# Optimization experiments

Measured on AMD Instinct MI355X. Metric: run time of the kernel, lower is better.

Reference implementation:

```python
import jax, jax.numpy as jnp
import numpy as np

B_, L_, D_MODEL = 2, 2048, 1024
D_INNER, D_STATE, D_CONV, DT_RANK = 2048, 16, 4, 64


def setup_inputs() -> dict:
    key = jax.random.key(0)
    ks = jax.random.split(key, 8)
    hidden_states = jax.random.normal(ks[0], (B_, L_, D_MODEL), jnp.float32)
    in_proj_w = jax.random.normal(ks[1], (2 * D_INNER, D_MODEL), jnp.float32) * (D_MODEL ** -0.5)
    conv_w = jax.random.normal(ks[2], (D_INNER, 1, D_CONV), jnp.float32) * (D_CONV ** -0.5)
    conv_b = jnp.zeros((D_INNER,), jnp.float32)
    x_proj_w = jax.random.normal(ks[3], (DT_RANK + 2 * D_STATE, D_INNER), jnp.float32) * (D_INNER ** -0.5)
    dt_std = DT_RANK ** -0.5
    dt_proj_w = jax.random.uniform(ks[4], (D_INNER, DT_RANK), jnp.float32, -dt_std, dt_std)
    # softplus-inverse init for dt bias, dt ~ loguniform[1e-3, 1e-1]
    dt = jnp.exp(jax.random.uniform(ks[5], (D_INNER,), jnp.float32)
                 * (np.log(0.1) - np.log(0.001)) + np.log(0.001))
    dt_proj_b = dt + jnp.log(-jnp.expm1(-dt))
    A_log = jnp.log(jnp.broadcast_to(jnp.arange(1, D_STATE + 1, dtype=jnp.float32), (D_INNER, D_STATE)))
    D = jnp.ones((D_INNER,), jnp.float32)
    out_proj_w = jax.random.normal(ks[6], (D_MODEL, D_INNER), jnp.float32) * (D_INNER ** -0.5)
    return dict(hidden_states=hidden_states, in_proj_w=in_proj_w, conv_w=conv_w,
                conv_b=conv_b, x_proj_w=x_proj_w, dt_proj_w=dt_proj_w,
                dt_proj_b=dt_proj_b, A_log=A_log, D=D, out_proj_w=out_proj_w)


def _mamba(hidden_states, in_proj_w, conv_w, conv_b, x_proj_w, dt_proj_w,
           dt_proj_b, A_log, D, out_proj_w):
    B, L, _ = hidden_states.shape
    # in_proj: (B,L,D) -> (B, 2*d_inner, L)
    xz = jnp.einsum('bld,ed->bel', hidden_states, in_proj_w)
    x, z = jnp.split(xz, 2, axis=1)  # each (B, d_inner, L)
    # causal depthwise conv1d (torch pads d_conv-1 both sides then truncates to L == left pad only)
    xp = jnp.pad(x, ((0, 0), (0, 0), (D_CONV - 1, 0)))
    xc = jax.lax.conv_general_dilated(xp, conv_w, (1,), 'VALID',
                                      dimension_numbers=('NCH', 'OIH', 'NCH'),
                                      feature_group_count=D_INNER)
    x = jax.nn.silu(xc + conv_b[None, :, None])  # (B, d_inner, L)
    # x_proj -> dt, B, C
    x_dbl = jnp.einsum('bdl,kd->bkl', x, x_proj_w)  # (B, dt_rank+2n, L)
    dt_in = x_dbl[:, :DT_RANK]
    Bm = x_dbl[:, DT_RANK:DT_RANK + D_STATE]   # (B, n, L)
    Cm = x_dbl[:, DT_RANK + D_STATE:]          # (B, n, L)
    delta = jnp.einsum('brl,dr->bdl', dt_in, dt_proj_w)
    delta = jax.nn.softplus(delta + dt_proj_b[None, :, None])  # (B, d_inner, L)
    A = -jnp.exp(A_log)  # (d_inner, n)
    # discretize: dA (L,B,d,n), dBu (L,B,d,n)
    dA = jnp.exp(jnp.einsum('bdl,dn->lbdn', delta, A))
    dBu = jnp.einsum('bdl,bnl,bdl->lbdn', delta, Bm, x)
    C_t = jnp.transpose(Cm, (2, 0, 1))  # (L, B, n)

    def step(h, inp):
        dA_t, dBu_t, c_t = inp
        h = dA_t * h + dBu_t                       # (B, d_inner, n)
        y = jnp.einsum('bdn,bn->bd', h, c_t)
        return h, y

    h0 = jnp.zeros((B, D_INNER, D_STATE), delta.dtype)
    _, ys = jax.lax.scan(step, h0, (dA, dBu, C_t))  # ys: (L, B, d_inner)
    y = jnp.transpose(ys, (1, 2, 0))                # (B, d_inner, L)
    y = y + x * D[None, :, None]
    y = y * jax.nn.silu(z)
    return jnp.einsum('bdl,od->blo', y, out_proj_w)  # (B, L, d_model)


def reference(hidden_states, in_proj_w, conv_w, conv_b, x_proj_w, dt_proj_w,
              dt_proj_b, A_log, D, out_proj_w):
    return _mamba(hidden_states, in_proj_w, conv_w, conv_b, x_proj_w,
                  dt_proj_w, dt_proj_b, A_log, D, out_proj_w)
```

## Files before the change

### kernel.cpp

```cpp
#include <hip/hip_runtime.h>
#include <hip/hip_bf16.h>

#define B_    2
#define L_    2048
#define DM_   1024
#define DI_   2048
#define DS_   16
#define DTR_  64
#define KC_   8

typedef __bf16 v8bf __attribute__((ext_vector_type(8)));
typedef float  v4f  __attribute__((ext_vector_type(4)));
typedef unsigned short us8 __attribute__((ext_vector_type(8)));

__device__ __forceinline__ unsigned cvt_pk_bf16(float lo, float hi) {
  unsigned r;
  asm("v_cvt_pk_bf16_f32 %0, %1, %2" : "=v"(r) : "v"(lo), "v"(hi));
  return r;
}

template<int CTRL>
__device__ __forceinline__ float dpp_shr_add(float x) {
  int xi = __builtin_bit_cast(int, x);
  int yi = __builtin_amdgcn_update_dpp(xi, xi, CTRL, 0xF, 0xF, true);
  return x + __builtin_bit_cast(float, yi);
}

template<int BCOL, int CT>
__global__ __launch_bounds__(256) void gemm_mfma(
    const float* __restrict__ A, const float* __restrict__ B,
    float* __restrict__ C,
    int M, int N, int K, int lda, int ldb, int ldc,
    long long sA, long long sB_, long long sC)
{
  __shared__ unsigned short lA[128 * 32];
  __shared__ unsigned short lB[128 * 32];

  const int tid  = threadIdx.x;
  const int bz   = blockIdx.z;
  A += sA  * bz;
  B += sB_ * bz;
  C += sC  * bz;

  const int m0 = blockIdx.y * 128;
  const int n0 = blockIdx.x * 128;
  const int wave = tid >> 6, lane = tid & 63;
  const int wr = wave >> 1, wc = wave & 1;
  const int lrow = lane & 15, lk = lane >> 4;

  v4f acc[4][4];
  #pragma unroll
  for (int i = 0; i < 4; ++i)
    #pragma unroll
    for (int j = 0; j < 4; ++j) acc[i][j] = (v4f)0.f;

  const int sr  = tid >> 1, skh = (tid & 1) * 16;
  const int cn4 = (tid & 31) * 4, ck4 = (tid >> 5) * 4;

  for (int k0 = 0; k0 < K; k0 += 32) {
    __syncthreads();
    {
      const float* src = A + (long long)(m0 + sr) * lda + k0 + skh;
      unsigned t32[8];
      #pragma unroll
      for (int q = 0; q < 4; ++q) {
        float4 v = *(const float4*)(src + q * 4);
        t32[2*q]   = cvt_pk_bf16(v.x, v.y);
        t32[2*q+1] = cvt_pk_bf16(v.z, v.w);
      }
      int b0 = sr * 64 + skh * 2;
      int sw = (sr & 7) << 4;
      *(uint4*)((char*)lA + ((b0)      ^ sw)) = *(uint4*)&t32[0];
      *(uint4*)((char*)lA + ((b0 + 16) ^ sw)) = *(uint4*)&t32[4];
    }
    if (BCOL == 0) {
      const float* src = B + (long long)(n0 + sr) * ldb + k0 + skh;
      unsigned t32[8];
      #pragma unroll
      for (int q = 0; q < 4; ++q) {
        float4 v = *(const float4*)(src + q * 4);
        t32[2*q]   = cvt_pk_bf16(v.x, v.y);
        t32[2*q+1] = cvt_pk_bf16(v.z, v.w);
      }
      int b0 = sr * 64 + skh * 2;
      int sw = (sr & 7) << 4;
      *(uint4*)((char*)lB + ((b0)      ^ sw)) = *(uint4*)&t32[0];
      *(uint4*)((char*)lB + ((b0 + 16) ^ sw)) = *(uint4*)&t32[4];
    } else {
      float va[4][4];
      #pragma unroll
      for (int kk = 0; kk < 4; ++kk) {
        float4 v = *(const float4*)(B + (long long)(k0 + ck4 + kk) * ldb + n0 + cn4);
        va[kk][0] = v.x; va[kk][1] = v.y; va[kk][2] = v.z; va[kk][3] = v.w;
      }
      #pragma unroll
      for (int nn = 0; nn < 4; ++nn) {
        unsigned w01 = cvt_pk_bf16(va[0][nn], va[1][nn]);
        unsigned w23 = cvt_pk_bf16(va[2][nn], va[3][nn]);
        int row = cn4 + nn;
        int b0  = row * 64 + ck4 * 2;
        unsigned* dst = (unsigned*)((char*)lB + (b0 ^ ((row & 7) << 4)));
        dst[0] = w01;
        dst[1] = w23;
      }
    }
    __syncthreads();

    v8bf af[4], bf[4];
    #pragma unroll
    for (int i = 0; i < 4; ++i) {
      int r  = wr * 64 + i * 16 + lrow;
      int b0 = (r * 64 + lk * 16) ^ ((r & 7) << 4);
      af[i] = __builtin_bit_cast(v8bf, *(const us8*)((const char*)lA + b0));
    }
    #pragma unroll
    for (int j = 0; j < 4; ++j) {
      int r  = wc * 64 + j * 16 + lrow;
      int b0 = (r * 64 + lk * 16) ^ ((r & 7) << 4);
      bf[j] = __builtin_bit_cast(v8bf, *(const us8*)((const char*)lB + b0));
    }
    #pragma unroll
    for (int i = 0; i < 4; ++i)
      #pragma unroll
      for (int j = 0; j < 4; ++j)
        acc[i][j] = __builtin_amdgcn_mfma_f32_16x16x32_bf16(af[i], bf[j], acc[i][j], 0, 0, 0);
  }

  #pragma unroll
  for (int i = 0; i < 4; ++i) {
    #pragma unroll
    for (int j = 0; j < 4; ++j) {
      int gm = m0 + wr * 64 + i * 16 + lk * 4;
      int gn = n0 + wc * 64 + j * 16 + lrow;
      if (CT == 0) {
        #pragma unroll
        for (int r = 0; r < 4; ++r)
          C[(long long)(gm + r) * ldc + gn] = acc[i][j][r];
      } else {
        *(v4f*)&C[(long long)gn * ldc + gm] = acc[i][j];
      }
    }
  }
}

template<int AMODE, int BMODE, int ACT>
__global__ __launch_bounds__(256) void gemm64(
    const float* __restrict__ A, const float* __restrict__ B,
    float* __restrict__ C, const float* __restrict__ bias,
    int M, int N, int K, int lda, int ldb, int ldc,
    long long sA, long long sB_, long long sC)
{
  constexpr int BM = 64, BN = 64, BK = 16;
  __shared__ float As[BK][BM + 4];
  __shared__ float Bs[BK][BN + 4];

  const int tid = threadIdx.x;
  const int bz  = blockIdx.z;
  A += sA  * bz;
  B += sB_ * bz;
  C += sC  * bz;

  const int m0 = blockIdx.y * BM;
  const int n0 = blockIdx.x * BN;
  const int tx = tid & 15;
  const int ty = tid >> 4;

  float acc[4][4] = {};

  for (int k0 = 0; k0 < K; k0 += BK) {
    #pragma unroll
    for (int i = 0; i < 4; ++i) {
      int idx = tid + i * 256;
      int m, k;
      if (AMODE == 0) { k = idx & (BK - 1); m = idx >> 4; }
      else            { m = idx & (BM - 1); k = idx >> 6; }
      int gm = m0 + m;
      float v = 0.f;
      if (gm < M)
        v = (AMODE == 0) ? A[(long long)gm * lda + (k0 + k)]
                         : A[(long long)(k0 + k) * lda + gm];
      As[k][m] = v;
    }
    #pragma unroll
    for (int i = 0; i < 4; ++i) {
      int idx = tid + i * 256;
      int n, k;
      if (BMODE == 0) { k = idx & (BK - 1); n = idx >> 4; }
      else            { n = idx & (BN - 1); k = idx >> 6; }
      int gn = n0 + n;
      float v = (BMODE == 0) ? B[(long long)gn * ldb + (k0 + k)]
                             : B[(long long)(k0 + k) * ldb + gn];
      Bs[k][n] = v;
    }
    __syncthreads();

    #pragma unroll
    for (int k = 0; k < BK; ++k) {
      float4 av = *(const float4*)&As[k][ty * 4];
      float4 bv = *(const float4*)&Bs[k][tx * 4];
      float a_[4] = {av.x, av.y, av.z, av.w};
      float b_[4] = {bv.x, bv.y, bv.z, bv.w};
      #pragma unroll
      for (int i = 0; i < 4; ++i)
        #pragma unroll
        for (int j = 0; j < 4; ++j)
          acc[i][j] = fmaf(a_[i], b_[j], acc[i][j]);
    }
    __syncthreads();
  }

  #pragma unroll
  for (int i = 0; i < 4; ++i) {
    int gm = m0 + ty * 4 + i;
    if (gm < M) {
      float bv = (ACT == 1) ? bias[gm] : 0.f;
      #pragma unroll
      for (int j = 0; j < 4; ++j) {
        float v = acc[i][j];
        if (ACT == 1) {
          v += bv;
          v = (v > 20.f) ? v : __logf(1.f + __expf(v));
        }
        C[(long long)gm * ldc + n0 + tx * 4 + j] = v;
      }
    }
  }
}

__global__ __launch_bounds__(256) void gemm64_p(
    const float* __restrict__ A, const float* __restrict__ B,
    float* __restrict__ part,
    int M, int N, int K, int lda, int ldb,
    long long sB_)
{
  constexpr int BM = 64, BN = 64, BK = 16;
  __shared__ float As[BK][BM + 4];
  __shared__ float Bs[BK][BN + 4];

  const int tid = threadIdx.x;
  const int bz  = blockIdx.z;
  B += sB_ * bz;

  const int m0  = (blockIdx.y & 1) * BM;
  const int kc  = blockIdx.y >> 1;
  const int n0  = blockIdx.x * BN;
  const int kend = (kc + 1) * (K / KC_);
  const int tx = tid & 15;
  const int ty = tid >> 4;

  float* Cp = part + ((size_t)(kc * B_ + bz) * 96) * (size_t)L_;

  float acc[4][4] = {};

  for (int k0 = kc * (K / KC_); k0 < kend; k0 += BK) {
    #pragma unroll
    for (int i = 0; i < 4; ++i) {
      int idx = tid + i * 256;
      int k = idx & (BK - 1), m = idx >> 4;
      int gm = m0 + m;
      As[k][m] = (gm < M) ? A[(long long)gm * lda + (k0 + k)] : 0.f;
    }
    #pragma unroll
    for (int i = 0; i < 4; ++i) {
      int idx = tid + i * 256;
      int n = idx & (BN - 1), k = idx >> 6;
      Bs[k][n] = B[(long long)(k0 + k) * ldb + (n0 + n)];
    }
    __syncthreads();

    #pragma unroll
    for (int k = 0; k < BK; ++k) {
      float4 av = *(const float4*)&As[k][ty * 4];
      float4 bv = *(const float4*)&Bs[k][tx * 4];
      float a_[4] = {av.x, av.y, av.z, av.w};
      float b_[4] = {bv.x, bv.y, bv.z, bv.w};
      #pragma unroll
      for (int i = 0; i < 4; ++i)
        #pragma unroll
        for (int j = 0; j < 4; ++j)
          acc[i][j] = fmaf(a_[i], b_[j], acc[i][j]);
    }
    __syncthreads();
  }

  #pragma unroll
  for (int i = 0; i < 4; ++i) {
    int gm = m0 + ty * 4 + i;
    if (gm < M)
      *(float4*)&Cp[(size_t)gm * L_ + n0 + tx * 4] = *(float4*)&acc[i][0];
  }
}

__global__ __launch_bounds__(256) void k3_reduce(
    const float* __restrict__ part, float* __restrict__ xdbl)
{
  int i   = blockIdx.x * 256 + threadIdx.x;
  int l4  = (i & (L_ / 4 - 1)) << 2;
  int row = i >> 9;
  float4 a = make_float4(0.f, 0.f, 0.f, 0.f);
  #pragma unroll
  for (int kc = 0; kc < KC_; ++kc) {
    float4 v = *(const float4*)&part[((size_t)(kc * B_ * 96 + row)) * L_ + l4];
    a.x += v.x; a.y += v.y; a.z += v.z; a.w += v.w;
  }
  *(float4*)&xdbl[(size_t)row * L_ + l4] = a;
}

__global__ __launch_bounds__(256) void conv_silu_kernel(
    const float* __restrict__ xz, const float* __restrict__ cw,
    const float* __restrict__ cb, float* __restrict__ xc)
{
  int idx = blockIdx.x * 256 + threadIdx.x;
  int l4  = (idx & (L_ / 4 - 1)) << 2;
  int row = idx >> 9;
  int d   = row & (DI_ - 1);
  int b   = row >> 11;

  const float* in = xz + ((size_t)b * 2 * DI_ + d) * L_;
  float w0 = cw[d * 4 + 0], w1 = cw[d * 4 + 1];
  float w2 = cw[d * 4 + 2], w3 = cw[d * 4 + 3];
  float bias = cb[d];

  float o[4];
  #pragma unroll
  for (int j = 0; j < 4; ++j) {
    int l = l4 + j;
    float acc = bias + in[l] * w3;
    if (l >= 1) acc += in[l - 1] * w2;
    if (l >= 2) acc += in[l - 2] * w1;
    if (l >= 3) acc += in[l - 3] * w0;
    float sig = 1.f / (1.f + __expf(-acc));
    o[j] = acc * sig;
  }
  *(float4*)&xc[(size_t)row * L_ + l4] = *(float4*)o;
}

__global__ __launch_bounds__(256) void gate_silu_kernel(float* __restrict__ xz)
{
  int idx = blockIdx.x * 256 + threadIdx.x;
  int l4  = (idx & (L_ / 4 - 1)) << 2;
  int row = idx >> 9;
  int d   = row & (DI_ - 1);
  int b   = row >> 11;

  float*       y = xz + ((size_t)b * 2 * DI_ + d) * L_;
  const float* z = xz + ((size_t)b * 2 * DI_ + DI_ + d) * L_;

  float4 yv = *(const float4*)&y[l4];
  float4 zv = *(const float4*)&z[l4];
  float o[4] = {yv.x, yv.y, yv.z, yv.w};
  float zz[4] = {zv.x, zv.y, zv.z, zv.w};
  #pragma unroll
  for (int j = 0; j < 4; ++j) {
    float sig = 1.f / (1.f + __expf(-zz[j]));
    o[j] = o[j] * zz[j] * sig;
  }
  *(float4*)&y[l4] = *(const float4*)o;
}

__global__ __launch_bounds__(256) void scan_kernel(
    float* __restrict__ xz, const float* __restrict__ xconv,
    const float* __restrict__ x_dbl, const float* __restrict__ A_log,
    const float* __restrict__ Dw)
{
  const int tid = threadIdx.x;
  const int g   = tid >> 4;
  const int n   = tid & 15;
  const int gid = blockIdx.x * 16 + g;
  const int b   = gid >> 11;
  const int d   = gid & (DI_ - 1);
  const int bb  = blockIdx.x >> 7;

  const float An = -expf(A_log[d * DS_ + n]);
  const float Dd = Dw[d];

  const float* drow = xz    + ((size_t)b * 2 * DI_ + d) * L_;
  const float* xrow = xconv + ((size_t)b * DI_ + d) * L_;
  float*       yrow = xz    + ((size_t)b * 2 * DI_ + d) * L_;

  const float* Bbase = x_dbl + ((size_t)bb * 96 + DTR_) * L_;
  const float* Cbase = x_dbl + ((size_t)bb * 96 + DTR_ + DS_) * L_;

  __shared__ float sB[2][16][68], sC[2][16][68];

  const int sr = tid >> 4, sc4 = (tid & 15) * 4;
  const size_t soff = (size_t)sr * L_ + sc4;

  float4 rB = *(const float4*)&Bbase[soff];
  float4 rC = *(const float4*)&Cbase[soff];

  float4 nD0 = *(const float4*)&drow[0], nD1 = *(const float4*)&drow[4];
  float4 nX0 = *(const float4*)&xrow[0], nX1 = *(const float4*)&xrow[4];

  float h = 0.f;
  int cur = 0;
  for (int l0 = 0; l0 < L_; l0 += 64) {
    *(float4*)&sB[cur][sr][sc4] = rB;
    *(float4*)&sC[cur][sr][sc4] = rC;
    if (l0 + 64 < L_) {
      rB = *(const float4*)&Bbase[soff + l0 + 64];
      rC = *(const float4*)&Cbase[soff + l0 + 64];
    }
    __syncthreads();

    #pragma unroll
    for (int l8 = 0; l8 < 64; l8 += 8) {
      const int l = l0 + l8;
      float dv[8], xv[8], Bn[8], Cn[8];
      *(float4*)&dv[0] = nD0; *(float4*)&dv[4] = nD1;
      *(float4*)&xv[0] = nX0; *(float4*)&xv[4] = nX1;

      if (l + 8 < L_) {
        nD0 = *(const float4*)&drow[l + 8]; nD1 = *(const float4*)&drow[l + 12];
        nX0 = *(const float4*)&xrow[l + 8]; nX1 = *(const float4*)&xrow[l + 12];
      }

      *(float4*)&Bn[0] = *(const float4*)&sB[cur][n][l8];
      *(float4*)&Bn[4] = *(const float4*)&sB[cur][n][l8 + 4];
      *(float4*)&Cn[0] = *(const float4*)&sC[cur][n][l8];
      *(float4*)&Cn[4] = *(const float4*)&sC[cur][n][l8 + 4];

      float dA[8], dBu[8];
      #pragma unroll
      for (int j = 0; j < 8; ++j) {
        dA[j]  = __expf(dv[j] * An);
        dBu[j] = dv[j] * Bn[j] * xv[j];
      }
      float p[8];
      #pragma unroll
      for (int j = 0; j < 8; ++j) {
        h = fmaf(dA[j], h, dBu[j]);
        p[j] = h * Cn[j];
      }
      #pragma unroll
      for (int j = 0; j < 8; ++j) p[j] = dpp_shr_add<0x111>(p[j]);
      #pragma unroll
      for (int j = 0; j < 8; ++j) p[j] = dpp_shr_add<0x112>(p[j]);
      #pragma unroll
      for (int j = 0; j < 8; ++j) p[j] = dpp_shr_add<0x114>(p[j]);
      #pragma unroll
      for (int j = 0; j < 8; ++j) p[j] = dpp_shr_add<0x118>(p[j]);

      if (n == 15) {
        float o[8];
        #pragma unroll
        for (int j = 0; j < 8; ++j)
          o[j] = p[j] + xv[j] * Dd;
        *(float4*)&yrow[l]     = *(const float4*)&o[0];
        *(float4*)&yrow[l + 4] = *(const float4*)&o[4];
      }
    }
    cur ^= 1;
  }
}

extern "C" void kernel_launch(void* const* d_in, const int* in_sizes, int n_in,
                              void* d_out, int out_size, void* d_ws, size_t ws_size,
                              hipStream_t stream)
{
  const float* hs   = (const float*)d_in[0];
  const float* w1   = (const float*)d_in[1];
  const float* cw   = (const float*)d_in[2];
  const float* cb   = (const float*)d_in[3];
  const float* xpw  = (const float*)d_in[4];
  const float* dtw  = (const float*)d_in[5];
  const float* dtbp = (const float*)d_in[6];
  const float* Alog = (const float*)d_in[7];
  const float* Dw   = (const float*)d_in[8];
  const float* wo   = (const float*)d_in[9];
  float* out = (float*)d_out;

  char* ws = (char*)d_ws;
  float* xz    = (float*)ws;
  float* xconv = (float*)(ws + (size_t)B_ * 2 * DI_ * L_ * 4);
  float* xdbl  = (float*)(ws + (size_t)B_ * 2 * DI_ * L_ * 4
                             + (size_t)B_ * DI_ * L_ * 4);

  float* part = xz;

  {
    dim3 g(L_ / 128, (2 * DI_) / 128, B_);
    gemm_mfma<0, 0><<<g, 256, 0, stream>>>(w1, hs, xz,
        2 * DI_, L_, DM_, DM_, DM_, L_,
        0LL, (long long)L_ * DM_, (long long)2 * DI_ * L_);
  }

  conv_silu_kernel<<<dim3(B_ * DI_ * L_ / 4 / 256), 256, 0, stream>>>(xz, cw, cb, xconv);

  {
    dim3 g(L_ / 64, 2 * KC_, B_);
    gemm64_p<<<g, 256, 0, stream>>>(xpw, xconv, part,
        96, L_, DI_, DI_, L_,
        (long long)DI_ * L_);
  }
  k3_reduce<<<dim3(B_ * 96 * L_ / 4 / 256), 256, 0, stream>>>(part, xdbl);

  {
    dim3 g(L_ / 64, DI_ / 64, B_);
    gemm64<0, 1, 1><<<g, 256, 0, stream>>>(dtw, xdbl, xz, dtbp,
        DI_, L_, DTR_, DTR_, L_, L_,
        0LL, (long long)96 * L_, (long long)2 * DI_ * L_);
  }

  scan_kernel<<<dim3(B_ * DI_ / 16), 256, 0, stream>>>(xz, xconv, xdbl, Alog, Dw);

  gate_silu_kernel<<<dim3(B_ * DI_ * L_ / 4 / 256), 256, 0, stream>>>(xz);

  {
    dim3 g(L_ / 128, DM_ / 128, B_);
    gemm_mfma<1, 1><<<g, 256, 0, stream>>>(wo, xz, out,
        DM_, L_, DI_, DI_, L_, DM_,
        0LL, (long long)2 * DI_ * L_, (long long)L_ * DM_);
  }
}
```

Measured before the change: 386.9 us.

## Transpose B/C into interleaved per-timestep layout and drop LDS staging in scan

Adds a small kernel that transposes the B and C rows of x_dbl into an (L, n, 2) interleaved layout, written into the already-consumed dt region of the workspace. The scan kernel then loads each lane's (B,C) pair straight from global memory with prefetched float2 loads. This removes the shared-memory double buffer and the per-64-step __syncthreads from the scan. The cost is an extra kernel launch plus more global load instructions per step, which rely on cache reuse across the 16-lane groups.

```diff
diff --git a/kernel.cpp b/kernel.cpp
--- a/kernel.cpp
+++ b/kernel.cpp
@@ -306,6 +306,39 @@
   *(float4*)&xdbl[(size_t)row * L_ + l4] = a;
 }
 
+__global__ __launch_bounds__(256) void bc_transpose(
+    const float* __restrict__ xdbl, float* __restrict__ BCt)
+{
+  const int b  = blockIdx.y;
+  const int l0 = blockIdx.x * 64;
+  const int t  = threadIdx.x;
+  __shared__ float st[32][65];
+
+  {
+    int r = t >> 3, c8 = (t & 7) * 8;
+    const float* src = xdbl + ((size_t)(b * 96 + DTR_ + r)) * L_ + l0 + c8;
+    float4 a = *(const float4*)src;
+    float4 c = *(const float4*)(src + 4);
+    st[r][c8+0] = a.x; st[r][c8+1] = a.y; st[r][c8+2] = a.z; st[r][c8+3] = a.w;
+    st[r][c8+4] = c.x; st[r][c8+5] = c.y; st[r][c8+6] = c.z; st[r][c8+7] = c.w;
+  }
+  __syncthreads();
+
+  {
+    int lc = t >> 2, q4 = (t & 3) * 4;
+    int l  = l0 + lc;
+    float o[8];
+    #pragma unroll
+    for (int i = 0; i < 4; ++i) {
+      o[2*i]   = st[q4 + i][lc];
+      o[2*i+1] = st[16 + q4 + i][lc];
+    }
+    float* dst = BCt + ((size_t)b * L_ + l) * 32 + q4 * 2;
+    *(float4*)dst       = *(const float4*)&o[0];
+    *(float4*)(dst + 4) = *(const float4*)&o[4];
+  }
+}
+
 __global__ __launch_bounds__(256) void conv_silu_kernel(
     const float* __restrict__ xz, const float* __restrict__ cw,
     const float* __restrict__ cb, float* __restrict__ xc)
@@ -360,7 +393,7 @@
 
 __global__ __launch_bounds__(256) void scan_kernel(
     float* __restrict__ xz, const float* __restrict__ xconv,
-    const float* __restrict__ x_dbl, const float* __restrict__ A_log,
+    const float* __restrict__ BCt, const float* __restrict__ A_log,
     const float* __restrict__ Dw)
 {
   const int tid = threadIdx.x;
@@ -369,7 +402,6 @@
   const int gid = blockIdx.x * 16 + g;
   const int b   = gid >> 11;
   const int d   = gid & (DI_ - 1);
-  const int bb  = blockIdx.x >> 7;
 
   const float An = -expf(A_log[d * DS_ + n]);
   const float Dd = Dw[d];
@@ -377,80 +409,59 @@
   const float* drow = xz    + ((size_t)b * 2 * DI_ + d) * L_;
   const float* xrow = xconv + ((size_t)b * DI_ + d) * L_;
   float*       yrow = xz    + ((size_t)b * 2 * DI_ + d) * L_;
-
-  const float* Bbase = x_dbl + ((size_t)bb * 96 + DTR_) * L_;
-  const float* Cbase = x_dbl + ((size_t)bb * 96 + DTR_ + DS_) * L_;
-
-  __shared__ float sB[2][16][68], sC[2][16][68];
-
-  const int sr = tid >> 4, sc4 = (tid & 15) * 4;
-  const size_t soff = (size_t)sr * L_ + sc4;
-
-  float4 rB = *(const float4*)&Bbase[soff];
-  float4 rC = *(const float4*)&Cbase[soff];
+  const float* bc   = BCt + ((size_t)b * L_ * 16 + n) * 2;
 
   float4 nD0 = *(const float4*)&drow[0], nD1 = *(const float4*)&drow[4];
   float4 nX0 = *(const float4*)&xrow[0], nX1 = *(const float4*)&xrow[4];
+  float2 nBC[8];
+  #pragma unroll
+  for (int j = 0; j < 8; ++j) nBC[j] = *(const float2*)&bc[j * 32];
 
   float h = 0.f;
-  int cur = 0;
-  for (int l0 = 0; l0 < L_; l0 += 64) {
-    *(float4*)&sB[cur][sr][sc4] = rB;
-    *(float4*)&sC[cur][sr][sc4] = rC;
-    if (l0 + 64 < L_) {
-      rB = *(const float4*)&Bbase[soff + l0 + 64];
-      rC = *(const float4*)&Cbase[soff + l0 + 64];
-    }
-    __syncthreads();
-
-    #pragma unroll
-    for (int l8 = 0; l8 < 64; l8 += 8) {
-      const int l = l0 + l8;
-      float dv[8], xv[8], Bn[8], Cn[8];
-      *(float4*)&dv[0] = nD0; *(float4*)&dv[4] = nD1;
-      *(float4*)&xv[0] = nX0; *(float4*)&xv[4] = nX1;
-
-      if (l + 8 < L_) {
-        nD0 = *(const float4*)&drow[l + 8]; nD1 = *(const float4*)&drow[l + 12];
-        nX0 = *(const float4*)&xrow[l + 8]; nX1 = *(const float4*)&xrow[l + 12];
-      }
-
-      *(float4*)&Bn[0] = *(const float4*)&sB[cur][n][l8];
-      *(float4*)&Bn[4] = *(const float4*)&sB[cur][n][l8 + 4];
-      *(float4*)&Cn[0] = *(const float4*)&sC[cur][n][l8];
-      *(float4*)&Cn[4] = *(const float4*)&sC[cur][n][l8 + 4];
-
-      float dA[8], dBu[8];
-      #pragma unroll
-      for (int j = 0; j < 8; ++j) {
-        dA[j]  = __expf(dv[j] * An);
-        dBu[j] = dv[j] * Bn[j] * xv[j];
-      }
-      float p[8];
-      #pragma unroll
-      for (int j = 0; j < 8; ++j) {
-        h = fmaf(dA[j], h, dBu[j]);
-        p[j] = h * Cn[j];
-      }
-      #pragma unroll
-      for (int j = 0; j < 8; ++j) p[j] = dpp_shr_add<0x111>(p[j]);
-      #pragma unroll
-      for (int j = 0; j < 8; ++j) p[j] = dpp_shr_add<0x112>(p[j]);
-      #pragma unroll
-      for (int j = 0; j < 8; ++j) p[j] = dpp_shr_add<0x114>(p[j]);
-      #pragma unroll
-      for (int j = 0; j < 8; ++j) p[j] = dpp_shr_add<0x118>(p[j]);
-
-      if (n == 15) {
-        float o[8];
-        #pragma unroll
-        for (int j = 0; j < 8; ++j)
-          o[j] = p[j] + xv[j] * Dd;
-        *(float4*)&yrow[l]     = *(const float4*)&o[0];
-        *(float4*)&yrow[l + 4] = *(const float4*)&o[4];
-      }
-    }
-    cur ^= 1;
+  for (int l8 = 0; l8 < L_; l8 += 8) {
+    float dv[8], xv[8];
+    float2 bcv[8];
+    *(float4*)&dv[0] = nD0; *(float4*)&dv[4] = nD1;
+    *(float4*)&xv[0] = nX0; *(float4*)&xv[4] = nX1;
+    #pragma unroll
+    for (int j = 0; j < 8; ++j) bcv[j] = nBC[j];
+
+    if (l8 + 8 < L_) {
+      nD0 = *(const float4*)&drow[l8 + 8]; nD1 = *(const float4*)&drow[l8 + 12];
+      nX0 = *(const float4*)&xrow[l8 + 8]; nX1 = *(const float4*)&xrow[l8 + 12];
+      #pragma unroll
+      for (int j = 0; j < 8; ++j) nBC[j] = *(const float2*)&bc[(l8 + 8 + j) * 32];
+    }
+
+    float dA[8], dBu[8];
+    #pragma unroll
+    for (int j = 0; j < 8; ++j) {
+      dA[j]  = __expf(dv[j] * An);
+      dBu[j] = dv[j] * bcv[j].x * xv[j];
+    }
+    float p[8];
+    #pragma unroll
+    for (int j = 0; j < 8; ++j) {
+      h = fmaf(dA[j], h, dBu[j]);
+      p[j] = h * bcv[j].y;
+    }
+    #pragma unroll
+    for (int j = 0; j < 8; ++j) p[j] = dpp_shr_add<0x111>(p[j]);
+    #pragma unroll
+    for (int j = 0; j < 8; ++j) p[j] = dpp_shr_add<0x112>(p[j]);
+    #pragma unroll
+    for (int j = 0; j < 8; ++j) p[j] = dpp_shr_add<0x114>(p[j]);
+    #pragma unroll
+    for (int j = 0; j < 8; ++j) p[j] = dpp_shr_add<0x118>(p[j]);
+
+    if (n == 15) {
+      float o[8];
+      #pragma unroll
+      for (int j = 0; j < 8; ++j)
+        o[j] = p[j] + xv[j] * Dd;
+      *(float4*)&yrow[l8]     = *(const float4*)&o[0];
+      *(float4*)&yrow[l8 + 4] = *(const float4*)&o[4];
+    }
   }
 }
 
@@ -477,6 +488,7 @@
                              + (size_t)B_ * DI_ * L_ * 4);
 
   float* part = xz;
+  float* BCt = xdbl;
 
   {
     dim3 g(L_ / 128, (2 * DI_) / 128, B_);
@@ -502,7 +514,9 @@
         0LL, (long long)96 * L_, (long long)2 * DI_ * L_);
   }
 
-  scan_kernel<<<dim3(B_ * DI_ / 16), 256, 0, stream>>>(xz, xconv, xdbl, Alog, Dw);
+  bc_transpose<<<dim3(L_ / 64, B_), 256, 0, stream>>>(xdbl, BCt);
+
+  scan_kernel<<<dim3(B_ * DI_ / 16), 256, 0, stream>>>(xz, xconv, BCt, Alog, Dw);
 
   gate_silu_kernel<<<dim3(B_ * DI_ * L_ / 4 / 256), 256, 0, stream>>>(xz);
 
```

New measurement: 444.6 us. 14.9% more time.
